# Kernel tuning notes

Hardware: AMD Instinct MI355X
Metric: run time of the kernel (lower is better)

## Reference

```python
import jax, jax.numpy as jnp
import numpy as np

B_SZ, N, NX, NU, NY, NW = 128, 2048, 64, 32, 64, 64


def setup_inputs() -> dict:
    key = jax.random.key(0)
    ks = jax.random.split(key, 10)
    sx = 1.0 / np.sqrt(NX)
    su = 1.0 / np.sqrt(NU)
    sw = 1.0 / np.sqrt(NW)
    return {
        "x0": jax.random.normal(ks[0], (B_SZ, NX), jnp.float32),
        "us": jax.random.normal(ks[1], (B_SZ, N, NU), jnp.float32),
        # state matrix scaled for (approximate) stability of the recurrence
        "A": 0.9 * sx * jax.random.normal(ks[2], (NX, NX), jnp.float32),
        "B1": su * jax.random.normal(ks[3], (NX, NU), jnp.float32),
        "B2": sw * jax.random.normal(ks[4], (NX, NW), jnp.float32),
        "C1": sx * jax.random.normal(ks[5], (NY, NX), jnp.float32),
        "D11": su * jax.random.normal(ks[6], (NY, NU), jnp.float32),
        "D12": sw * jax.random.normal(ks[7], (NY, NW), jnp.float32),
        "C2": sx * jax.random.normal(ks[8], (NW, NX), jnp.float32),
        "D21": su * jax.random.normal(ks[9], (NW, NU), jnp.float32),
    }


def reference(x0, us, A, B1, B2, C1, D11, D12, C2, D21):
    """LureSystem.forward: sequential Lure recurrence with tanh nonlinearity.

    x0: [B, nx], us: [B, N, nu] -> ys: [B, N, ny]
    Per step k (matching torch: x is updated BEFORE computing y_k):
      w = tanh(C2 x + D21 u_k)
      x <- A x + B1 u_k + B2 w
      y_k = C1 x + D11 u_k + D12 w
    """
    def step(x, u):
        w = jnp.tanh(x @ C2.T + u @ D21.T)          # [B, nw]
        x_next = x @ A.T + u @ B1.T + w @ B2.T      # [B, nx]
        y = x_next @ C1.T + u @ D11.T + w @ D12.T   # [B, ny]
        return x_next, y

    us_t = jnp.swapaxes(us, 0, 1)                    # [N, B, nu]
    _, ys_t = jax.lax.scan(step, x0, us_t)           # ys_t: [N, B, ny]
    return jnp.swapaxes(ys_t, 0, 1)                  # [B, N, ny]
```

## Files before the change

kernel.cpp:

```cpp
#include <hip/hip_runtime.h>


#define NT 2048

typedef __attribute__((ext_vector_type(8))) short short8;
typedef __attribute__((ext_vector_type(4))) float f4;
typedef __attribute__((ext_vector_type(2))) int i2;

union Frag { int i[4]; i2 h[2]; short8 v; };

__device__ __forceinline__ unsigned rne_bf16(float f) {
  unsigned u = __float_as_uint(f);
  return (u + 0x7FFFu + ((u >> 16) & 1u)) >> 16;
}
__device__ __forceinline__ void split2(float a, float b, int& hi, int& lo) {
  unsigned ha = rne_bf16(a), hb = rne_bf16(b);
  float ra = a - __uint_as_float(ha << 16);
  float rb = b - __uint_as_float(hb << 16);
  hi = (int)(ha | (hb << 16));
  lo = (int)(rne_bf16(ra) | (rne_bf16(rb) << 16));
}
__device__ __forceinline__ void split8(const float* x, Frag& hi, Frag& lo) {
#pragma unroll
  for (int p = 0; p < 4; p++) split2(x[2 * p], x[2 * p + 1], hi.i[p], lo.i[p]);
}
__device__ __forceinline__ int cvtpk(float a, float b) {
  int r;
  asm("v_cvt_pk_bf16_f32 %0, %1, %2" : "=v"(r) : "v"(a), "v"(b));
  return r;
}
__device__ __forceinline__ void split2c(float a, float b, int& hi, int& lo) {
  hi = cvtpk(a, b);
  float ra = a - __uint_as_float((unsigned)hi << 16);
  float rb = b - __uint_as_float((unsigned)hi & 0xFFFF0000u);
  lo = cvtpk(ra, rb);
}
__device__ __forceinline__ float ftanh(float x) {
  float e = __expf(2.0f * x);
  return 1.0f - 2.0f * __builtin_amdgcn_rcpf(e + 1.0f);
}
__device__ __forceinline__ f4 mf(const Frag& a, const Frag& b, f4 c) {
  return __builtin_amdgcn_mfma_f32_16x16x32_bf16(a.v, b.v, c, 0, 0, 0);
}
__device__ __forceinline__ float ror8f(float x) {
  return __int_as_float(
      __builtin_amdgcn_mov_dpp(__float_as_int(x), 0x128, 0xf, 0xf, true));
}
__device__ __forceinline__ void lds_barrier() {
  __builtin_amdgcn_s_waitcnt(0xC07F);
  __builtin_amdgcn_s_barrier();
}
__device__ __forceinline__ void wfrag(const float* W, int row0, int c, int lane,
                                      Frag& hi, Frag& lo) {
  const int m = lane & 15, qq = lane >> 4;
  const f4* p = (const f4*)(W + (size_t)(row0 + m) * 192 + 32 * c + 8 * qq);
  f4 a = p[0], b = p[1];
  float t[8] = {a[0], a[1], a[2], a[3], b[0], b[1], b[2], b[3]};
  split8(t, hi, lo);
}

__global__ void prep_w(const float* __restrict__ A, const float* __restrict__ B1,
                       const float* __restrict__ B2, const float* __restrict__ C1,
                       const float* __restrict__ D11, const float* __restrict__ D12,
                       const float* __restrict__ C2, const float* __restrict__ D21,
                       float* __restrict__ Wfull) {
  const int r = blockIdx.x;
  const int c = threadIdx.x;
  float v = 0.f;
  if (c < 64) {
    const int j = c;
    if (r < 64) v = A[r * 64 + j];
    else if (r < 128) { float s = 0.f; for (int l = 0; l < 64; l++) s += C2[(r - 64) * 64 + l] * A[l * 64 + j]; v = s; }
    else { float s = 0.f; for (int l = 0; l < 64; l++) s += C1[(r - 128) * 64 + l] * A[l * 64 + j]; v = s; }
  } else if (c < 128) {
    const int j = c - 64;
    if (r < 64) v = B2[r * 64 + j];
    else if (r < 128) { float s = 0.f; for (int l = 0; l < 64; l++) s += C2[(r - 64) * 64 + l] * B2[l * 64 + j]; v = s; }
    else { float s = 0.f; for (int l = 0; l < 64; l++) s += C1[(r - 128) * 64 + l] * B2[l * 64 + j]; v = s + D12[(r - 128) * 64 + j]; }
  } else if (c < 160) {
    const int j = c - 128;
    if (r < 64) v = B1[r * 32 + j];
    else if (r < 128) { float s = 0.f; for (int l = 0; l < 64; l++) s += C2[(r - 64) * 64 + l] * B1[l * 32 + j]; v = s; }
    else { float s = 0.f; for (int l = 0; l < 64; l++) s += C1[(r - 128) * 64 + l] * B1[l * 32 + j]; v = s + D11[(r - 128) * 32 + j]; }
  } else {
    const int j = c - 160;
    v = (r >= 64 && r < 128) ? D21[(r - 64) * 32 + j] : 0.f;
  }
  Wfull[r * 192 + c] = v;
}

__global__ __launch_bounds__(256)
void prep_uu(const float* __restrict__ us, const float* __restrict__ Wfull,
             float* __restrict__ UU) {
  const int blk = blockIdx.x;
  const int kc = blockIdx.y;
  const int wv = threadIdx.x >> 6;
  const int lane = threadIdx.x & 63;
  const int nn = lane & 15, q = lane >> 4;
  const int b0 = blk * 16;

  Frag zh4, zl4, zh5, zl5, xh4, xl4, yh4, yl4;
  wfrag(Wfull, 64 + 16 * wv, 4, lane, zh4, zl4);
  wfrag(Wfull, 64 + 16 * wv, 5, lane, zh5, zl5);
  wfrag(Wfull, 16 * wv, 4, lane, xh4, xl4);
  wfrag(Wfull, 128 + 16 * wv, 4, lane, yh4, yl4);

  const float* ubase = us + (size_t)(b0 + nn) * (NT * 32) + 8 * q;
  int k = kc * 32;
  Frag uhc, ulc, uhn, uln;
  {
    const f4* p = (const f4*)(ubase + (size_t)k * 32);
    f4 a = p[0], b = p[1];
    float t[8] = {a[0], a[1], a[2], a[3], b[0], b[1], b[2], b[3]};
    split8(t, uhc, ulc);
  }
  f4 ra, rb;
  {
    const int kn = (k + 1 < NT) ? k + 1 : NT - 1;
    const f4* p = (const f4*)(ubase + (size_t)kn * 32);
    ra = p[0]; rb = p[1];
  }
  for (int k0 = 0; k0 < 32; k0++, k++) {
    {
      float t[8] = {ra[0], ra[1], ra[2], ra[3], rb[0], rb[1], rb[2], rb[3]};
      split8(t, uhn, uln);
    }
    {
      const int kp = (k + 2 < NT) ? k + 2 : NT - 1;
      const f4* p = (const f4*)(ubase + (size_t)kp * 32);
      ra = p[0]; rb = p[1];
    }
    f4 az = {0.f, 0.f, 0.f, 0.f}, ax = az, ay = az;
    az = mf(zh4, uhc, az); az = mf(zh5, uhn, az);
    az = mf(zh4, ulc, az); az = mf(zh5, uln, az);
    az = mf(zl4, uhc, az); az = mf(zl5, uhn, az);
    ax = mf(xh4, uhc, ax); ax = mf(xh4, ulc, ax); ax = mf(xl4, uhc, ax);
    ay = mf(yh4, uhc, ay); ay = mf(yh4, ulc, ay); ay = mf(yl4, uhc, ay);
    float* dst = UU + ((size_t)k * 8 + blk) * 3072 + lane * 4;
    *(f4*)(dst + wv * 256) = az;
    *(f4*)(dst + (4 + wv) * 256) = ax;
    *(f4*)(dst + (8 + wv) * 256) = ay;
    uhc = uhn; ulc = uln;
  }
}

__global__ __launch_bounds__(512, 1)
void lure_fused(const float* __restrict__ x0, const float* __restrict__ us,
                const float* __restrict__ C2, const float* __restrict__ D21,
                const float* __restrict__ Wfull, float* __restrict__ UU,
                float* __restrict__ out, unsigned* done) {
  __shared__ int lds[2][4][272];
  const int tid = threadIdx.x;

  if (blockIdx.x >= 16) {
    const int stride = (gridDim.x - 16) * 2;
    const int unit = (blockIdx.x - 16) * 2 + (tid >> 8);
    const int t2 = tid & 255;
    const int wv = t2 >> 6;
    const int lane = t2 & 63;
    const int nn = lane & 15, q = lane >> 4;

    Frag zh4, zl4, zh5, zl5, xh4, xl4, yh4, yl4;
    wfrag(Wfull, 64 + 16 * wv, 4, lane, zh4, zl4);
    wfrag(Wfull, 64 + 16 * wv, 5, lane, zh5, zl5);
    wfrag(Wfull, 16 * wv, 4, lane, xh4, xl4);
    wfrag(Wfull, 128 + 16 * wv, 4, lane, yh4, yl4);

    for (int tile = unit; tile < 512; tile += stride) {
      const int blk = tile & 7, kc = tile >> 3;
      const int b0 = blk * 16;
      const float* ubase = us + (size_t)(b0 + nn) * (NT * 32) + 8 * q;
      int k = kc * 32;
      Frag uhc, ulc, uhn, uln;
      {
        const f4* p = (const f4*)(ubase + (size_t)k * 32);
        f4 a = p[0], b = p[1];
        float tt[8] = {a[0], a[1], a[2], a[3], b[0], b[1], b[2], b[3]};
        split8(tt, uhc, ulc);
      }
      f4 ra, rb;
      {
        const int kn = (k + 1 < NT) ? k + 1 : NT - 1;
        const f4* p = (const f4*)(ubase + (size_t)kn * 32);
        ra = p[0]; rb = p[1];
      }
      for (int k0 = 0; k0 < 32; k0++, k++) {
        {
          float tt[8] = {ra[0], ra[1], ra[2], ra[3], rb[0], rb[1], rb[2], rb[3]};
          split8(tt, uhn, uln);
        }
        {
          const int kp = (k + 2 < NT) ? k + 2 : NT - 1;
          const f4* p = (const f4*)(ubase + (size_t)kp * 32);
          ra = p[0]; rb = p[1];
        }
        f4 az = {0.f, 0.f, 0.f, 0.f}, ax = az, ay = az;
        az = mf(zh4, uhc, az); az = mf(zh5, uhn, az);
        az = mf(zh4, ulc, az); az = mf(zh5, uln, az);
        az = mf(zl4, uhc, az); az = mf(zl5, uhn, az);
        ax = mf(xh4, uhc, ax); ax = mf(xh4, ulc, ax); ax = mf(xl4, uhc, ax);
        ay = mf(yh4, uhc, ay); ay = mf(yh4, ulc, ay); ay = mf(yl4, uhc, ay);
        float* dst = UU + ((size_t)k * 8 + blk) * 3072 + lane * 4;
        *(f4*)(dst + wv * 256) = az;
        *(f4*)(dst + (4 + wv) * 256) = ax;
        *(f4*)(dst + (8 + wv) * 256) = ay;
        uhc = uhn; ulc = uln;
      }
    }
    __syncthreads();
    __threadfence();
    if (done && tid == 0) atomicAdd(done, 1u);
    return;
  }

  const int wave = tid >> 6;
  const int lane = tid & 63;
  const int q = lane >> 4;
  const int nn = lane & 15;
  const int b8 = blockIdx.x * 8;
  const int ro = q * 68 + nn * 4;
  const size_t KSTRIDE = 8 * 12 * 256;
  const int ob = blockIdx.x >> 1, hh = blockIdx.x & 1;
  const int ulane = 8 * hh + (lane & 7) + 16 * q;
  const float msk = (lane & 8) ? 0.f : 1.f;

  if (tid < 128) {
    const int n = tid >> 4;
    const int f0 = (tid & 15) * 4;
    const int c = f0 >> 5;
    const int g = (f0 & 31) >> 3;
    const int d = (f0 & 7) >> 1;
    const int idx = g * 68 + n * 4 + d;
    const float* xrow = x0 + (b8 + n) * 64;
    float xv[4] = {xrow[f0], xrow[f0 + 1], xrow[f0 + 2], xrow[f0 + 3]};
    int h0, l0, h1, l1;
    split2(xv[0], xv[1], h0, l0);
    split2(xv[2], xv[3], h1, l1);
    lds[0][c][idx] = h0;       lds[0][c][idx + 1] = h1;
    lds[0][c][idx + 32] = l0;  lds[0][c][idx + 33] = l1;
    float zv[4] = {0.f, 0.f, 0.f, 0.f};
    for (int j = 0; j < 64; j++) {
      float xj = xrow[j];
#pragma unroll
      for (int r = 0; r < 4; r++) zv[r] += C2[(f0 + r) * 64 + j] * xj;
    }
    const float* urow = us + (size_t)(b8 + n) * (NT * 32);
    for (int j = 0; j < 32; j++) {
      float uj = urow[j];
#pragma unroll
      for (int r = 0; r < 4; r++) zv[r] += D21[(f0 + r) * 32 + j] * uj;
    }
#pragma unroll
    for (int r = 0; r < 4; r++) zv[r] = ftanh(zv[r]);
    split2(zv[0], zv[1], h0, l0);
    split2(zv[2], zv[3], h1, l1);
    lds[0][2 + c][idx] = h0;       lds[0][2 + c][idx + 1] = h1;
    lds[0][2 + c][idx + 32] = l0;  lds[0][2 + c][idx + 33] = l1;
  }

  if (done != nullptr) {
    if (tid == 0) {
      const unsigned target = (unsigned)(gridDim.x - 16);
      while (__hip_atomic_load(done, __ATOMIC_ACQUIRE,
                               __HIP_MEMORY_SCOPE_AGENT) < target)
        __builtin_amdgcn_s_sleep(32);
    }
    __syncthreads();
  }

  if (wave < 4) {
    const int zt = wave;
    Frag WH[4], WL[4];
#pragma unroll
    for (int c = 0; c < 4; c++) wfrag(Wfull, 64 + 16 * zt, c, lane, WH[c], WL[c]);
    const float* up = UU + (((size_t)ob * 12 + zt) * 64 + ulane) * 4;
    f4 uz[4];
#pragma unroll
    for (int d = 0; d < 4; d++) uz[d] = *(const f4*)(up + (size_t)d * KSTRIDE);
    const int widx = (2 * (zt & 1) + (q >> 1)) * 68 + nn * 4 + 2 * (q & 1);
    const int rw = 2 + (zt >> 1);
    lds_barrier();

    auto zstep = [&](int kk, int d, int kp) {
      const int rb = kk & 1;
      Frag b[4];
#pragma unroll
      for (int c = 0; c < 4; c++) b[c].v = *(const short8*)&lds[rb][c][ro];
      f4 sA0 = {uz[d][0] * msk, uz[d][1] * msk, uz[d][2] * msk, uz[d][3] * msk};
      f4 z4 = {0.f, 0.f, 0.f, 0.f};
      f4 sA1 = z4, sB0 = z4, sB1 = z4;
      sA0 = mf(WH[0], b[0], sA0); sB0 = mf(WL[0], b[0], sB0);
      sA1 = mf(WH[1], b[1], sA1); sB1 = mf(WL[1], b[1], sB1);
      sA0 = mf(WH[2], b[2], sA0); sB0 = mf(WL[2], b[2], sB0);
      sA1 = mf(WH[3], b[3], sA1); sB1 = mf(WL[3], b[3], sB1);
      uz[d] = *(const f4*)(up + (size_t)kp * KSTRIDE);
      float wv[4];
#pragma unroll
      for (int r = 0; r < 4; r++) {
        float aa = sA0[r] + sA1[r];
        wv[r] = ftanh(aa + ror8f(aa) + (sB0[r] + sB1[r]));
      }
      int h0, l0, h1, l1;
      split2c(wv[0], wv[1], h0, l0);
      split2c(wv[2], wv[3], h1, l1);
      if ((lane & 8) == 0) {
        i2 wh; wh[0] = h0; wh[1] = h1;
        i2 wl; wl[0] = l0; wl[1] = l1;
        *(i2*)&lds[rb ^ 1][rw][widx] = wh;
        *(i2*)&lds[rb ^ 1][rw][widx + 32] = wl;
      }
      lds_barrier();
    };
    int k = 0;
    for (; k < NT - 4; k += 4) {
      zstep(k, 0, k + 4); zstep(k + 1, 1, k + 5);
      zstep(k + 2, 2, k + 6); zstep(k + 3, 3, k + 7);
    }
    zstep(k, 0, NT - 1); zstep(k + 1, 1, NT - 1);
    zstep(k + 2, 2, NT - 1); zstep(k + 3, 3, NT - 1);
  } else {
    const int xt = wave - 4;
    Frag WXH[4], WXL[4], WYH[4];
#pragma unroll
    for (int c = 0; c < 4; c++) {
      wfrag(Wfull, 16 * xt, c, lane, WXH[c], WXL[c]);
      Frag dmy;
      wfrag(Wfull, 128 + 16 * xt, c, lane, WYH[c], dmy);
    }
    const float* upx = UU + (((size_t)ob * 12 + 4 + xt) * 64 + ulane) * 4;
    const float* upy = UU + (((size_t)ob * 12 + 8 + xt) * 64 + ulane) * 4;
    f4 ux[4], uy[4];
#pragma unroll
    for (int d = 0; d < 4; d++) {
      ux[d] = *(const f4*)(upx + (size_t)d * KSTRIDE);
      uy[d] = *(const f4*)(upy + (size_t)d * KSTRIDE);
    }
    const int widx = (2 * (xt & 1) + (q >> 1)) * 68 + nn * 4 + 2 * (q & 1);
    const int rw = (xt >> 1);
    float* py0 = out + (size_t)(b8 + nn) * (NT * 64) + 16 * xt + 4 * q;
    lds_barrier();

    auto xstep = [&](int kk, int d, int kp) {
      const int rb = kk & 1;
      Frag b[4];
#pragma unroll
      for (int c = 0; c < 4; c++) b[c].v = *(const short8*)&lds[rb][c][ro];
      f4 tA0 = {ux[d][0] * msk, ux[d][1] * msk, ux[d][2] * msk, ux[d][3] * msk};
      f4 z4 = {0.f, 0.f, 0.f, 0.f};
      f4 tA1 = z4, tB0 = z4, tB1 = z4;
      f4 sy = uy[d];
      tA0 = mf(WXH[0], b[0], tA0); tB0 = mf(WXL[0], b[0], tB0);
      tA1 = mf(WXH[1], b[1], tA1); tB1 = mf(WXL[1], b[1], tB1);
      sy = mf(WYH[0], b[0], sy);   sy = mf(WYH[1], b[1], sy);
      tA0 = mf(WXH[2], b[2], tA0); tB0 = mf(WXL[2], b[2], tB0);
      tA1 = mf(WXH[3], b[3], tA1); tB1 = mf(WXL[3], b[3], tB1);
      sy = mf(WYH[2], b[2], sy);   sy = mf(WYH[3], b[3], sy);
      ux[d] = *(const f4*)(upx + (size_t)kp * KSTRIDE);
      uy[d] = *(const f4*)(upy + (size_t)kp * KSTRIDE);
      float xv[4];
#pragma unroll
      for (int r = 0; r < 4; r++) {
        float aa = tA0[r] + tA1[r];
        xv[r] = aa + ror8f(aa) + (tB0[r] + tB1[r]);
      }
      int h0, l0, h1, l1;
      split2c(xv[0], xv[1], h0, l0);
      split2c(xv[2], xv[3], h1, l1);
      if ((lane & 8) == 0) {
        i2 wh; wh[0] = h0; wh[1] = h1;
        i2 wl; wl[0] = l0; wl[1] = l1;
        *(i2*)&lds[rb ^ 1][rw][widx] = wh;
        *(i2*)&lds[rb ^ 1][rw][widx + 32] = wl;
        *(f4*)(py0 + (size_t)kk * 64) = sy;
      }
      lds_barrier();
    };
    int k = 0;
    for (; k < NT - 4; k += 4) {
      xstep(k, 0, k + 4); xstep(k + 1, 1, k + 5);
      xstep(k + 2, 2, k + 6); xstep(k + 3, 3, k + 7);
    }
    xstep(k, 0, NT - 1); xstep(k + 1, 1, NT - 1);
    xstep(k + 2, 2, NT - 1); xstep(k + 3, 3, NT - 1);
  }
}

__global__ __launch_bounds__(256, 1)
void lure_seq_fb(const float* __restrict__ x0, const float* __restrict__ us,
                 const float* __restrict__ C2, const float* __restrict__ D21,
                 const float* __restrict__ Wfull, float* __restrict__ out) {
  __shared__ int lds[2][8][272];
  const int tid = threadIdx.x;
  const int wave = tid >> 6;
  const int lane = tid & 63;
  const int q = lane >> 4;
  const int nn = lane & 15;
  const int b0 = blockIdx.x * 16;
  const int ro = q * 68 + nn * 4;
  {
    const int n = tid >> 4;
    const int f0 = (tid & 15) * 4;
    const int cc = f0 >> 5;
    const int g = (f0 & 31) >> 3;
    const int d = (f0 & 7) >> 1;
    const int idx = g * 68 + n * 4 + d;
    const float* xrow = x0 + (b0 + n) * 64;
    float xv[4] = {xrow[f0], xrow[f0 + 1], xrow[f0 + 2], xrow[f0 + 3]};
    int h0, l0, h1, l1;
    split2(xv[0], xv[1], h0, l0);
    split2(xv[2], xv[3], h1, l1);
    lds[0][cc][idx] = h0;     lds[0][cc][idx + 1] = h1;
    lds[0][2 + cc][idx] = l0; lds[0][2 + cc][idx + 1] = l1;
    float zv[4] = {0.f, 0.f, 0.f, 0.f};
    for (int j = 0; j < 64; j++) {
      float xj = xrow[j];
#pragma unroll
      for (int r = 0; r < 4; r++) zv[r] += C2[(f0 + r) * 64 + j] * xj;
    }
    const float* urow = us + (size_t)(b0 + n) * (NT * 32);
    for (int j = 0; j < 32; j++) {
      float uj = urow[j];
#pragma unroll
      for (int r = 0; r < 4; r++) zv[r] += D21[(f0 + r) * 32 + j] * uj;
    }
#pragma unroll
    for (int r = 0; r < 4; r++) zv[r] = ftanh(zv[r]);
    split2(zv[0], zv[1], h0, l0);
    split2(zv[2], zv[3], h1, l1);
    lds[0][4 + cc][idx] = h0; lds[0][4 + cc][idx + 1] = h1;
    lds[0][6 + cc][idx] = l0; lds[0][6 + cc][idx + 1] = l1;
  }
  Frag uh[2], ul[2];
  f4 ra0[4], ra1[4];
  const float* pu = us + ((size_t)(b0 + nn) * NT) * 32 + 8 * q;
#pragma unroll
  for (int j = 0; j < 2; j++) {
    const f4* p = (const f4*)(pu + j * 32);
    f4 a = p[0], b = p[1];
    float t[8] = {a[0], a[1], a[2], a[3], b[0], b[1], b[2], b[3]};
    split8(t, uh[j], ul[j]);
  }
#pragma unroll
  for (int j = 2; j <= 5; j++) {
    const f4* p = (const f4*)(pu + j * 32);
    ra0[j & 3] = p[0];
    ra1[j & 3] = p[1];
  }
  lds_barrier();

  if (wave < 2) {
    const int Z0 = wave * 2;
    Frag WH[2][6], WL[2][6];
#pragma unroll
    for (int t = 0; t < 2; t++)
#pragma unroll
      for (int c = 0; c < 6; c++)
        wfrag(Wfull, 64 + 16 * (Z0 + t), c, lane, WH[t][c], WL[t][c]);
    auto zstep = [&](int kk, int uu) {
      const int rb = uu & 1;
      Frag bh[4], bl[4];
#pragma unroll
      for (int c = 0; c < 4; c++) {
        const int s = (c < 2) ? c : 2 + c;
        bh[c].v = *(const short8*)&lds[rb][s][ro];
        bl[c].v = *(const short8*)&lds[rb][s + 2][ro];
      }
      const int i4 = uu & 1, i5 = (uu + 1) & 1;
#pragma unroll
      for (int t = 0; t < 2; t++) {
        f4 z4 = {0.f, 0.f, 0.f, 0.f};
        f4 s1a = z4, s1b = z4, s2a = z4, s2b = z4, s3a = z4, s3b = z4;
        s1a = mf(WH[t][0], bh[0], s1a); s1b = mf(WH[t][1], bh[1], s1b);
        s2a = mf(WH[t][0], bl[0], s2a); s2b = mf(WH[t][1], bl[1], s2b);
        s3a = mf(WL[t][0], bh[0], s3a); s3b = mf(WL[t][1], bh[1], s3b);
        s1a = mf(WH[t][2], bh[2], s1a); s1b = mf(WH[t][3], bh[3], s1b);
        s2a = mf(WH[t][2], bl[2], s2a); s2b = mf(WH[t][3], bl[3], s2b);
        s3a = mf(WL[t][2], bh[2], s3a); s3b = mf(WL[t][3], bh[3], s3b);
        s1a = mf(WH[t][4], uh[i4], s1a); s1b = mf(WH[t][5], uh[i5], s1b);
        s2a = mf(WH[t][4], ul[i4], s2a); s2b = mf(WH[t][5], ul[i5], s2b);
        s3a = mf(WL[t][4], uh[i4], s3a); s3b = mf(WL[t][5], uh[i5], s3b);
        float wv[4];
#pragma unroll
        for (int r = 0; r < 4; r++)
          wv[r] = ftanh(((s1a[r] + s1b[r]) + (s2a[r] + s2b[r])) + (s3a[r] + s3b[r]));
        int h0, l0, h1, l1;
        split2(wv[0], wv[1], h0, l0);
        split2(wv[2], wv[3], h1, l1);
        const int zt = Z0 + t;
        const int widx = (2 * (zt & 1) + (q >> 1)) * 68 + nn * 4 + 2 * (q & 1);
        i2 wh; wh[0] = h0; wh[1] = h1;
        i2 wl; wl[0] = l0; wl[1] = l1;
        *(i2*)&lds[rb ^ 1][4 + (zt >> 1)][widx] = wh;
        *(i2*)&lds[rb ^ 1][6 + (zt >> 1)][widx] = wl;
      }
      f4 a = ra0[(uu + 2) & 3], b = ra1[(uu + 2) & 3];
      float t8[8] = {a[0], a[1], a[2], a[3], b[0], b[1], b[2], b[3]};
      split8(t8, uh[uu & 1], ul[uu & 1]);
      const int kp = (kk + 6 < NT) ? kk + 6 : NT - 1;
      const f4* p = (const f4*)(pu + (size_t)kp * 32);
      ra0[(uu + 2) & 3] = p[0];
      ra1[(uu + 2) & 3] = p[1];
      lds_barrier();
    };
    for (int k = 0; k < NT; k += 4) {
      zstep(k, 0); zstep(k + 1, 1); zstep(k + 2, 2); zstep(k + 3, 3);
    }
  } else {
    const int X0 = (wave - 2) * 2;
    Frag WXH[2][5], WXL[2][5], WYH[2][5];
#pragma unroll
    for (int t = 0; t < 2; t++)
#pragma unroll
      for (int c = 0; c < 5; c++) {
        wfrag(Wfull, 16 * (X0 + t), c, lane, WXH[t][c], WXL[t][c]);
        Frag dmy;
        wfrag(Wfull, 128 + 16 * (X0 + t), c, lane, WYH[t][c], dmy);
      }
    float* py0 = out + (size_t)(b0 + nn) * (NT * 64) + 16 * X0 + 4 * q;
    auto xstep = [&](int kk, int uu) {
      const int rb = uu & 1;
      Frag bh[4], bl[4];
#pragma unroll
      for (int c = 0; c < 4; c++) {
        const int s = (c < 2) ? c : 2 + c;
        bh[c].v = *(const short8*)&lds[rb][s][ro];
        bl[c].v = *(const short8*)&lds[rb][s + 2][ro];
      }
      const int i4 = uu & 1;
#pragma unroll
      for (int t = 0; t < 2; t++) {
        f4 z4 = {0.f, 0.f, 0.f, 0.f};
        f4 s1 = z4, s2 = z4, s3 = z4, sy = z4;
#pragma unroll
        for (int c = 0; c < 4; c++) {
          s1 = mf(WXH[t][c], bh[c], s1);
          s2 = mf(WXH[t][c], bl[c], s2);
          s3 = mf(WXL[t][c], bh[c], s3);
          sy = mf(WYH[t][c], bh[c], sy);
        }
        s1 = mf(WXH[t][4], uh[i4], s1);
        s2 = mf(WXH[t][4], ul[i4], s2);
        s3 = mf(WXL[t][4], uh[i4], s3);
        sy = mf(WYH[t][4], uh[i4], sy);
        float xv[4];
#pragma unroll
        for (int r = 0; r < 4; r++) xv[r] = s1[r] + s2[r] + s3[r];
        int h0, l0, h1, l1;
        split2(xv[0], xv[1], h0, l0);
        split2(xv[2], xv[3], h1, l1);
        const int xt = X0 + t;
        const int widx = (2 * (xt & 1) + (q >> 1)) * 68 + nn * 4 + 2 * (q & 1);
        i2 wh; wh[0] = h0; wh[1] = h1;
        i2 wl; wl[0] = l0; wl[1] = l1;
        *(i2*)&lds[rb ^ 1][(xt >> 1)][widx] = wh;
        *(i2*)&lds[rb ^ 1][2 + (xt >> 1)][widx] = wl;
        *(f4*)(py0 + (size_t)kk * 64 + 16 * t) = sy;
      }
      f4 a = ra0[(uu + 2) & 3], b = ra1[(uu + 2) & 3];
      float t8[8] = {a[0], a[1], a[2], a[3], b[0], b[1], b[2], b[3]};
      split8(t8, uh[uu & 1], ul[uu & 1]);
      const int kp = (kk + 6 < NT) ? kk + 6 : NT - 1;
      const f4* p = (const f4*)(pu + (size_t)kp * 32);
      ra0[(uu + 2) & 3] = p[0];
      ra1[(uu + 2) & 3] = p[1];
      lds_barrier();
    };
    for (int k = 0; k < NT; k += 4) {
      xstep(k, 0); xstep(k + 1, 1); xstep(k + 2, 2); xstep(k + 3, 3);
    }
  }
}

extern "C" void kernel_launch(void* const* d_in, const int* in_sizes, int n_in,
                              void* d_out, int out_size, void* d_ws, size_t ws_size,
                              hipStream_t stream) {
  const float* x0  = (const float*)d_in[0];
  const float* us  = (const float*)d_in[1];
  const float* A   = (const float*)d_in[2];
  const float* B1  = (const float*)d_in[3];
  const float* B2  = (const float*)d_in[4];
  const float* C1  = (const float*)d_in[5];
  const float* D11 = (const float*)d_in[6];
  const float* D12 = (const float*)d_in[7];
  const float* C2  = (const float*)d_in[8];
  const float* D21 = (const float*)d_in[9];
  float* Wfull = (float*)d_ws;
  const size_t W_BYTES = (size_t)192 * 192 * 4;
  float* UU = (float*)((char*)d_ws + W_BYTES);
  const size_t UU_BYTES = (size_t)NT * 8 * 12 * 256 * 4;
  unsigned* flag = (unsigned*)((char*)d_ws + W_BYTES + UU_BYTES);
  float* out = (float*)d_out;

  prep_w<<<dim3(192), dim3(192), 0, stream>>>(A, B1, B2, C1, D11, D12, C2, D21, Wfull);
  if (ws_size >= W_BYTES + UU_BYTES + 256) {
    hipMemsetAsync(flag, 0, 256, stream);
    lure_fused<<<dim3(256), dim3(512), 0, stream>>>(x0, us, C2, D21, Wfull, UU,
                                                    out, flag);
  } else if (ws_size >= W_BYTES + UU_BYTES) {
    prep_uu<<<dim3(8, 64), dim3(256), 0, stream>>>(us, Wfull, UU);
    lure_fused<<<dim3(16), dim3(512), 0, stream>>>(x0, us, C2, D21, Wfull, UU,
                                                   out, nullptr);
  } else {
    lure_seq_fb<<<dim3(8), dim3(256), 0, stream>>>(x0, us, C2, D21, Wfull, out);
  }
}
```

Baseline: 1.058 ms.

## Gate sequential recurrence on per-chunk producer counters instead of a global wait

```diff
diff --git a/kernel.cpp b/kernel.cpp
--- a/kernel.cpp
+++ b/kernel.cpp
@@ -150,66 +150,94 @@
                 const float* __restrict__ Wfull, float* __restrict__ UU,
                 float* __restrict__ out, unsigned* done) {
   __shared__ int lds[2][4][272];
+  __shared__ int g_all;
   const int tid = threadIdx.x;
 
   if (blockIdx.x >= 16) {
-    const int stride = (gridDim.x - 16) * 2;
-    const int unit = (blockIdx.x - 16) * 2 + (tid >> 8);
-    const int t2 = tid & 255;
-    const int wv = t2 >> 6;
-    const int lane = t2 & 63;
+    const int w = tid >> 6;
+    const int lane = tid & 63;
     const int nn = lane & 15, q = lane >> 4;
-
-    Frag zh4, zl4, zh5, zl5, xh4, xl4, yh4, yl4;
-    wfrag(Wfull, 64 + 16 * wv, 4, lane, zh4, zl4);
-    wfrag(Wfull, 64 + 16 * wv, 5, lane, zh5, zl5);
-    wfrag(Wfull, 16 * wv, 4, lane, xh4, xl4);
-    wfrag(Wfull, 128 + 16 * wv, 4, lane, yh4, yl4);
-
-    for (int tile = unit; tile < 512; tile += stride) {
-      const int blk = tile & 7, kc = tile >> 3;
-      const int b0 = blk * 16;
-      const float* ubase = us + (size_t)(b0 + nn) * (NT * 32) + 8 * q;
-      int k = kc * 32;
-      Frag uhc, ulc, uhn, uln;
-      {
-        const f4* p = (const f4*)(ubase + (size_t)k * 32);
-        f4 a = p[0], b = p[1];
-        float tt[8] = {a[0], a[1], a[2], a[3], b[0], b[1], b[2], b[3]};
-        split8(tt, uhc, ulc);
-      }
-      f4 ra, rb;
-      {
-        const int kn = (k + 1 < NT) ? k + 1 : NT - 1;
-        const f4* p = (const f4*)(ubase + (size_t)kn * 32);
-        ra = p[0]; rb = p[1];
-      }
-      for (int k0 = 0; k0 < 32; k0++, k++) {
+    const int nw = (int)gridDim.x - 16;
+    if (w < 4) {
+      Frag zh4, zl4, zh5, zl5;
+      wfrag(Wfull, 64 + 16 * w, 4, lane, zh4, zl4);
+      wfrag(Wfull, 64 + 16 * w, 5, lane, zh5, zl5);
+      for (int tile = (int)blockIdx.x - 16; tile < 512; tile += nw) {
+        const int kc = tile >> 3, blk = tile & 7;
+        const float* ubase = us + (size_t)(blk * 16 + nn) * (NT * 32) + 8 * q;
+        int k = kc * 32;
+        Frag uhc, ulc, uhn, uln;
         {
-          float tt[8] = {ra[0], ra[1], ra[2], ra[3], rb[0], rb[1], rb[2], rb[3]};
-          split8(tt, uhn, uln);
+          const f4* p = (const f4*)(ubase + (size_t)k * 32);
+          f4 a = p[0], b = p[1];
+          float tt[8] = {a[0], a[1], a[2], a[3], b[0], b[1], b[2], b[3]};
+          split8(tt, uhc, ulc);
         }
+        f4 ra, rb;
         {
-          const int kp = (k + 2 < NT) ? k + 2 : NT - 1;
-          const f4* p = (const f4*)(ubase + (size_t)kp * 32);
+          const int kn = (k + 1 < NT) ? k + 1 : NT - 1;
+          const f4* p = (const f4*)(ubase + (size_t)kn * 32);
           ra = p[0]; rb = p[1];
         }
-        f4 az = {0.f, 0.f, 0.f, 0.f}, ax = az, ay = az;
-        az = mf(zh4, uhc, az); az = mf(zh5, uhn, az);
-        az = mf(zh4, ulc, az); az = mf(zh5, uln, az);
-        az = mf(zl4, uhc, az); az = mf(zl5, uhn, az);
-        ax = mf(xh4, uhc, ax); ax = mf(xh4, ulc, ax); ax = mf(xl4, uhc, ax);
-        ay = mf(yh4, uhc, ay); ay = mf(yh4, ulc, ay); ay = mf(yl4, uhc, ay);
-        float* dst = UU + ((size_t)k * 8 + blk) * 3072 + lane * 4;
-        *(f4*)(dst + wv * 256) = az;
-        *(f4*)(dst + (4 + wv) * 256) = ax;
-        *(f4*)(dst + (8 + wv) * 256) = ay;
-        uhc = uhn; ulc = uln;
-      }
-    }
-    __syncthreads();
-    __threadfence();
-    if (done && tid == 0) atomicAdd(done, 1u);
+        for (int k0 = 0; k0 < 32; k0++, k++) {
+          {
+            float tt[8] = {ra[0], ra[1], ra[2], ra[3], rb[0], rb[1], rb[2], rb[3]};
+            split8(tt, uhn, uln);
+          }
+          {
+            const int kp = (k + 2 < NT) ? k + 2 : NT - 1;
+            const f4* p = (const f4*)(ubase + (size_t)kp * 32);
+            ra = p[0]; rb = p[1];
+          }
+          f4 az = {0.f, 0.f, 0.f, 0.f};
+          az = mf(zh4, uhc, az); az = mf(zh5, uhn, az);
+          az = mf(zh4, ulc, az); az = mf(zh5, uln, az);
+          az = mf(zl4, uhc, az); az = mf(zl5, uhn, az);
+          *(f4*)(UU + ((size_t)k * 8 + blk) * 3072 + lane * 4 + w * 256) = az;
+          uhc = uhn; ulc = uln;
+        }
+        __syncthreads();
+        if (done && tid == 0) {
+          __threadfence();
+          atomicAdd(done + kc, 1u);
+          atomicAdd(done + 64, 1u);
+        }
+      }
+    } else {
+      const int wv = w - 4;
+      Frag xh4, xl4, yh4, yl4;
+      wfrag(Wfull, 16 * wv, 4, lane, xh4, xl4);
+      wfrag(Wfull, 128 + 16 * wv, 4, lane, yh4, yl4);
+      for (int tile = (int)blockIdx.x - 16; tile < 512; tile += nw) {
+        const int kc = tile >> 3, blk = tile & 7;
+        const float* ubase = us + (size_t)(blk * 16 + nn) * (NT * 32) + 8 * q;
+        int k = kc * 32;
+        f4 ra, rb;
+        {
+          const f4* p = (const f4*)(ubase + (size_t)k * 32);
+          ra = p[0]; rb = p[1];
+        }
+        for (int k0 = 0; k0 < 32; k0++, k++) {
+          Frag uhc, ulc;
+          {
+            float tt[8] = {ra[0], ra[1], ra[2], ra[3], rb[0], rb[1], rb[2], rb[3]};
+            split8(tt, uhc, ulc);
+          }
+          {
+            const int kp = (k + 1 < NT) ? k + 1 : NT - 1;
+            const f4* p = (const f4*)(ubase + (size_t)kp * 32);
+            ra = p[0]; rb = p[1];
+          }
+          f4 ax = {0.f, 0.f, 0.f, 0.f}, ay = ax;
+          ax = mf(xh4, uhc, ax); ax = mf(xh4, ulc, ax); ax = mf(xl4, uhc, ax);
+          ay = mf(yh4, uhc, ay); ay = mf(yh4, ulc, ay); ay = mf(yl4, uhc, ay);
+          float* dst = UU + ((size_t)k * 8 + blk) * 3072 + lane * 4;
+          *(f4*)(dst + (4 + wv) * 256) = ax;
+          *(f4*)(dst + (8 + wv) * 256) = ay;
+        }
+        __syncthreads();
+      }
+    }
     return;
   }
 
@@ -223,6 +251,26 @@
   const int ob = blockIdx.x >> 1, hh = blockIdx.x & 1;
   const int ulane = 8 * hh + (lane & 7) + 16 * q;
   const float msk = (lane & 8) ? 0.f : 1.f;
+
+  bool alldone = (done == nullptr);
+  auto gate = [&](int s) {
+    if (alldone) return;
+    if (tid == 0) {
+      unsigned tot;
+      for (;;) {
+        tot = __hip_atomic_load(done + 64, __ATOMIC_ACQUIRE,
+                                __HIP_MEMORY_SCOPE_AGENT);
+        if (tot >= 512u) break;
+        unsigned v = __hip_atomic_load(done + s, __ATOMIC_ACQUIRE,
+                                       __HIP_MEMORY_SCOPE_AGENT);
+        if (v >= 8u) break;
+        __builtin_amdgcn_s_sleep(8);
+      }
+      g_all = (tot >= 512u) ? 1 : 0;
+    }
+    __syncthreads();
+    if (g_all) alldone = true;
+  };
 
   if (tid < 128) {
     const int n = tid >> 4;
@@ -258,15 +306,7 @@
     lds[0][2 + c][idx + 32] = l0;  lds[0][2 + c][idx + 33] = l1;
   }
 
-  if (done != nullptr) {
-    if (tid == 0) {
-      const unsigned target = (unsigned)(gridDim.x - 16);
-      while (__hip_atomic_load(done, __ATOMIC_ACQUIRE,
-                               __HIP_MEMORY_SCOPE_AGENT) < target)
-        __builtin_amdgcn_s_sleep(32);
-    }
-    __syncthreads();
-  }
+  gate(0);
 
   if (wave < 4) {
     const int zt = wave;
@@ -313,6 +353,7 @@
     };
     int k = 0;
     for (; k < NT - 4; k += 4) {
+      if ((k & 31) == 28) gate((k + 4) >> 5);
       zstep(k, 0, k + 4); zstep(k + 1, 1, k + 5);
       zstep(k + 2, 2, k + 6); zstep(k + 3, 3, k + 7);
     }
@@ -377,6 +418,7 @@
     };
     int k = 0;
     for (; k < NT - 4; k += 4) {
+      if ((k & 31) == 28) gate((k + 4) >> 5);
       xstep(k, 0, k + 4); xstep(k + 1, 1, k + 5);
       xstep(k + 2, 2, k + 6); xstep(k + 3, 3, k + 7);
     }
@@ -592,8 +634,8 @@
   float* out = (float*)d_out;
 
   prep_w<<<dim3(192), dim3(192), 0, stream>>>(A, B1, B2, C1, D11, D12, C2, D21, Wfull);
-  if (ws_size >= W_BYTES + UU_BYTES + 256) {
-    hipMemsetAsync(flag, 0, 256, stream);
+  if (ws_size >= W_BYTES + UU_BYTES + 512) {
+    hipMemsetAsync(flag, 0, 512, stream);
     lure_fused<<<dim3(256), dim3(512), 0, stream>>>(x0, us, C2, D21, Wfull, UU,
                                                     out, flag);
   } else if (ws_size >= W_BYTES + UU_BYTES) {
```

Measured after the change: 990.3 us. -6.4%, faster.
